# Performance work log

Measured on AMD Instinct MI355X. Metric: run time of the kernel, lower is better.

Reference implementation:

```python
import jax, jax.numpy as jnp
import numpy as np

H = 96          # hidden_dim / GatedGraphConv out_channels
L = 6           # num_layers
F_IN = 32       # num_node_features
G = 4096        # number of graphs in batch
BN_EPS = 1e-5


def setup_inputs() -> dict:
    key = jax.random.key(0)
    ks = jax.random.split(key, 16)
    N, E = 100000, 400000
    x = jax.random.normal(ks[0], (N, F_IN), dtype=jnp.float32)
    edge_index = jax.random.randint(ks[1], (2, E), 0, N, dtype=jnp.int64)
    batch = jnp.sort(jax.random.randint(ks[2], (N,), 0, G, dtype=jnp.int64))
    s = 1.0 / np.sqrt(H)
    conv_w = jax.random.uniform(ks[3], (L, H, H), jnp.float32, -s, s)
    w_ih = jax.random.uniform(ks[4], (3 * H, H), jnp.float32, -s, s)
    w_hh = jax.random.uniform(ks[5], (3 * H, H), jnp.float32, -s, s)
    b_ih = jax.random.uniform(ks[6], (3 * H,), jnp.float32, -s, s)
    b_hh = jax.random.uniform(ks[7], (3 * H,), jnp.float32, -s, s)
    bn_gamma = jnp.ones((H,), jnp.float32)
    bn_beta = jnp.zeros((H,), jnp.float32)
    s1 = 1.0 / np.sqrt(H)
    fc1_w = jax.random.uniform(ks[8], (4 * H, H), jnp.float32, -s1, s1)
    fc1_b = jax.random.uniform(ks[9], (4 * H,), jnp.float32, -s1, s1)
    s2 = 1.0 / np.sqrt(4 * H)
    fc2_w = jax.random.uniform(ks[10], (H, 4 * H), jnp.float32, -s2, s2)
    fc2_b = jax.random.uniform(ks[11], (H,), jnp.float32, -s2, s2)
    fc3_w = jax.random.uniform(ks[12], (1, H), jnp.float32, -s1, s1)
    fc3_b = jax.random.uniform(ks[13], (1,), jnp.float32, -s1, s1)
    return dict(x=x, edge_index=edge_index, batch=batch, conv_w=conv_w,
                w_ih=w_ih, w_hh=w_hh, b_ih=b_ih, b_hh=b_hh,
                bn_gamma=bn_gamma, bn_beta=bn_beta,
                fc1_w=fc1_w, fc1_b=fc1_b, fc2_w=fc2_w, fc2_b=fc2_b,
                fc3_w=fc3_w, fc3_b=fc3_b)


def _gated_graph_conv(x, src, dst, conv_w, w_ih, w_hh, b_ih, b_hh):
    N = x.shape[0]
    # PyG zero-pads input features up to out_channels
    h = jnp.pad(x, ((0, 0), (0, H - x.shape[1])))
    for i in range(L):
        m = h @ conv_w[i]                         # [N, H]
        agg = jnp.zeros((N, H), m.dtype).at[dst].add(m[src])  # scatter-add at targets
        gi = agg @ w_ih.T + b_ih                  # [N, 3H]
        gh = h @ w_hh.T + b_hh                    # [N, 3H]
        i_r, i_z, i_n = jnp.split(gi, 3, axis=-1)
        h_r, h_z, h_n = jnp.split(gh, 3, axis=-1)
        r = jax.nn.sigmoid(i_r + h_r)
        z = jax.nn.sigmoid(i_z + h_z)
        n = jnp.tanh(i_n + r * h_n)
        h = (1.0 - z) * n + z * h
    return h


def reference(x, edge_index, batch, conv_w, w_ih, w_hh, b_ih, b_hh,
              bn_gamma, bn_beta, fc1_w, fc1_b, fc2_w, fc2_b, fc3_w, fc3_b):
    src, dst = edge_index[0], edge_index[1]
    h = _gated_graph_conv(x, src, dst, conv_w, w_ih, w_hh, b_ih, b_hh)
    h = jax.nn.relu(h)
    # global mean pool (dropout is identity in eval)
    sums = jax.ops.segment_sum(h, batch, num_segments=G)          # [G, H]
    counts = jax.ops.segment_sum(jnp.ones((h.shape[0],), h.dtype), batch, num_segments=G)
    pooled = sums / jnp.maximum(counts, 1.0)[:, None]
    # BatchNorm1d in eval mode: running_mean=0, running_var=1
    hbn = (pooled / jnp.sqrt(1.0 + BN_EPS)) * bn_gamma + bn_beta
    h1 = jax.nn.relu(hbn @ fc1_w.T + fc1_b)
    h2 = jax.nn.relu(h1 @ fc2_w.T + fc2_b)
    return h2 @ fc3_w.T + fc3_b                                    # [G, 1]
```

## Files before the change

kernel.cpp:

```cpp
#include <hip/hip_runtime.h>

#define H96 96
#define LAYERS 6
#define BN_EPS 1e-5f
#define SCAN_B 1024

typedef unsigned short u16;
typedef unsigned int u32;
typedef _Float16 f16;
typedef _Float16 h8 __attribute__((ext_vector_type(8)));
typedef float f32x4 __attribute__((ext_vector_type(4)));
typedef u32 u32x3 __attribute__((ext_vector_type(3)));

__device__ __forceinline__ float sigm(float x) { return 1.f / (1.f + __expf(-x)); }
__device__ __forceinline__ float tanh_(float x) { return 2.f / (1.f + __expf(-2.f * x)) - 1.f; }
__device__ __forceinline__ f32x4 splat4(float x) { f32x4 v = {x, x, x, x}; return v; }

struct h2s { f16 x, y; };

__device__ __forceinline__ void upk(u32 v, float& lo, float& hi) {
    union { u32 u; h2s h; } c;
    c.u = v;
    lo = (float)c.h.x;
    hi = (float)c.h.y;
}

__global__ void k_f2h(const float* __restrict__ convw, const float* __restrict__ wih,
                      const float* __restrict__ whh, const float* __restrict__ fc1w,
                      const float* __restrict__ fc2w, f16* __restrict__ dst) {
    int i = blockIdx.x * 256 + threadIdx.x;
    if (i >= 184320) return;
    float v;
    if (i < 55296) v = convw[i];
    else if (i < 82944) v = wih[i - 55296];
    else if (i < 110592) v = whh[i - 82944];
    else if (i < 147456) v = fc1w[i - 110592];
    else v = fc2w[i - 147456];
    dst[i] = (f16)v;
}

__global__ __launch_bounds__(256) void k_wpt(const f16* __restrict__ wih16, const f16* __restrict__ convw16,
                                             f16* __restrict__ wpt) {
    int l = blockIdx.y;
    int lane = threadIdx.x & 63, wave = threadIdx.x >> 6;
    int l15 = lane & 15, q = lane >> 4;
    int rowa = blockIdx.x * 64 + wave * 16 + l15;
    if (rowa >= 288) rowa = 287;
    const f16* B = convw16 + (size_t)l * 9216;
    h8 af[3];
#pragma unroll
    for (int s = 0; s < 3; s++) af[s] = *(const h8*)(wih16 + (size_t)rowa * 96 + s * 32 + q * 8);
    f32x4 acc[6];
#pragma unroll
    for (int t = 0; t < 6; t++) acc[t] = splat4(0.f);
#pragma unroll
    for (int s = 0; s < 3; s++)
#pragma unroll
        for (int t = 0; t < 6; t++) {
            h8 b = *(const h8*)(B + (size_t)(t * 16 + l15) * 96 + s * 32 + q * 8);
            acc[t] = __builtin_amdgcn_mfma_f32_16x16x32_f16(af[s], b, acc[t], 0, 0, 0);
        }
    int rbase = blockIdx.x * 64 + wave * 16 + q * 4;
#pragma unroll
    for (int t = 0; t < 6; t++)
#pragma unroll
        for (int rr = 0; rr < 4; rr++) {
            int row = rbase + rr;
            if (row < 288) wpt[(size_t)l * 27648 + (size_t)row * 96 + t * 16 + l15] = (f16)acc[t][rr];
        }
}

__global__ void k_pad(const float* __restrict__ x, f16* __restrict__ hf, int N) {
    int i = blockIdx.x * 256 + threadIdx.x;
    if (i >= N * H96) return;
    int n = i / H96, c = i - n * H96;
    float v = (c < 32) ? x[n * 32 + c] : 0.f;
    hf[i] = (f16)v;
}

__global__ void k_hist(const int* __restrict__ key, int* __restrict__ deg, int E) {
    int e = blockIdx.x * 256 + threadIdx.x;
    if (e < E) atomicAdd(&deg[key[e]], 1);
}

__global__ __launch_bounds__(SCAN_B) void k_scan1(const int* __restrict__ deg, int* __restrict__ incl,
                                                  int* __restrict__ bsum, int N) {
    __shared__ int sh[SCAN_B];
    int i = blockIdx.x * SCAN_B + threadIdx.x;
    int v = (i < N) ? deg[i] : 0;
    sh[threadIdx.x] = v;
    __syncthreads();
    for (int off = 1; off < SCAN_B; off <<= 1) {
        int t = (threadIdx.x >= (u32)off) ? sh[threadIdx.x - off] : 0;
        __syncthreads();
        sh[threadIdx.x] += t;
        __syncthreads();
    }
    incl[blockIdx.x * SCAN_B + threadIdx.x] = sh[threadIdx.x];
    if (threadIdx.x == SCAN_B - 1) bsum[blockIdx.x] = sh[threadIdx.x];
}

__global__ void k_scan2(int* __restrict__ bsum, int nb) {
    if (blockIdx.x == 0 && threadIdx.x == 0) {
        int run = 0;
        for (int i = 0; i < nb; i++) { run += bsum[i]; bsum[i] = run; }
    }
}

__global__ void k_scan3(const int* __restrict__ deg, const int* __restrict__ incl, const int* __restrict__ bsum,
                        int* __restrict__ rs, int* __restrict__ cur, int N, int E) {
    int i = blockIdx.x * 256 + threadIdx.x;
    if (i == 0) rs[N] = E;
    if (i < N) {
        int b = i / SCAN_B;
        int off = (b > 0) ? bsum[b - 1] : 0;
        int ex = incl[i] - deg[i] + off;
        rs[i] = ex;
        if (cur) cur[i] = ex;
    }
}

__global__ void k_fill(const int* __restrict__ src, const int* __restrict__ dst, int* __restrict__ cur,
                       int* __restrict__ es, int E) {
    int e = blockIdx.x * 256 + threadIdx.x;
    if (e < E) {
        int p = atomicAdd(&cur[dst[e]], 1);
        es[p] = src[e];
    }
}

__global__ __launch_bounds__(256) void k_gather(const f16* __restrict__ hin, const int* __restrict__ rs,
                                                const int* __restrict__ es, f16* __restrict__ agg, int N) {
    int grp = threadIdx.x >> 4;
    int lane6 = threadIdx.x & 15;
    int node = blockIdx.x * 16 + grp;
    if (node >= N) return;
    int s = rs[node], e = rs[node + 1];
    float a0 = 0, a1 = 0, a2 = 0, a3 = 0, a4 = 0, a5 = 0;
    const char* basep = (const char*)hin;
    int off = lane6 * 12;
    for (int i = s; i < e; i += 4) {
        int j1 = (i + 1 < e) ? i + 1 : i;
        int j2 = (i + 2 < e) ? i + 2 : i;
        int j3 = (i + 3 < e) ? i + 3 : i;
        float m1 = (i + 1 < e) ? 1.f : 0.f;
        float m2 = (i + 2 < e) ? 1.f : 0.f;
        float m3 = (i + 3 < e) ? 1.f : 0.f;
        int sa = es[i], sb = es[j1], sc = es[j2], sd = es[j3];
        u32x3 va = *(const u32x3*)(basep + (size_t)sa * 192 + off);
        u32x3 vb = *(const u32x3*)(basep + (size_t)sb * 192 + off);
        u32x3 vc = *(const u32x3*)(basep + (size_t)sc * 192 + off);
        u32x3 vd = *(const u32x3*)(basep + (size_t)sd * 192 + off);
        float t0, t1;
        upk(va.x, t0, t1); a0 += t0; a1 += t1;
        upk(va.y, t0, t1); a2 += t0; a3 += t1;
        upk(va.z, t0, t1); a4 += t0; a5 += t1;
        upk(vb.x, t0, t1); a0 += t0 * m1; a1 += t1 * m1;
        upk(vb.y, t0, t1); a2 += t0 * m1; a3 += t1 * m1;
        upk(vb.z, t0, t1); a4 += t0 * m1; a5 += t1 * m1;
        upk(vc.x, t0, t1); a0 += t0 * m2; a1 += t1 * m2;
        upk(vc.y, t0, t1); a2 += t0 * m2; a3 += t1 * m2;
        upk(vc.z, t0, t1); a4 += t0 * m2; a5 += t1 * m2;
        upk(vd.x, t0, t1); a0 += t0 * m3; a1 += t1 * m3;
        upk(vd.y, t0, t1); a2 += t0 * m3; a3 += t1 * m3;
        upk(vd.z, t0, t1); a4 += t0 * m3; a5 += t1 * m3;
    }
    f16* dp = agg + (size_t)node * H96 + lane6 * 6;
    h2s p0, p1, p2;
    p0.x = (f16)a0; p0.y = (f16)a1;
    p1.x = (f16)a2; p1.y = (f16)a3;
    p2.x = (f16)a4; p2.y = (f16)a5;
    *(h2s*)(dp + 0) = p0;
    *(h2s*)(dp + 2) = p1;
    *(h2s*)(dp + 4) = p2;
}

__global__ __launch_bounds__(384, 4) void k_gru(const f16* __restrict__ agg, const f16* __restrict__ hin,
                                                f16* __restrict__ hout, const f16* __restrict__ wpt,
                                                const f16* __restrict__ whh, const float* __restrict__ bih,
                                                const float* __restrict__ bhh, int N) {
    int w = threadIdx.x >> 6;
    int lane = threadIdx.x & 63;
    int l15 = lane & 15, q = lane >> 4;
    int jr = w * 16 + l15;
    float b_r = bih[jr] + bhh[jr];
    float b_z = bih[96 + jr] + bhh[96 + jr];
    float b_in = bih[192 + jr];
    float b_hn = bhh[192 + jr];
    h8 wr0[3], wr1[3], wz0[3], wz1[3], wn0[3], wn1[3];
#pragma unroll
    for (int s = 0; s < 3; s++) {
        int ko = s * 32 + q * 8;
        wr0[s] = *(const h8*)(wpt + (size_t)jr * H96 + ko);
        wz0[s] = *(const h8*)(wpt + (size_t)(96 + jr) * H96 + ko);
        wn0[s] = *(const h8*)(wpt + (size_t)(192 + jr) * H96 + ko);
        wr1[s] = *(const h8*)(whh + (size_t)jr * H96 + ko);
        wz1[s] = *(const h8*)(whh + (size_t)(96 + jr) * H96 + ko);
        wn1[s] = *(const h8*)(whh + (size_t)(192 + jr) * H96 + ko);
    }
    int ntiles = (N + 15) >> 4;
    for (int tile = blockIdx.x; tile < ntiles; tile += gridDim.x) {
        int base = tile << 4;
        int rowa = base + l15;
        if (rowa >= N) rowa = N - 1;
        h8 as_[3], ah[3];
#pragma unroll
        for (int s = 0; s < 3; s++) {
            as_[s] = *(const h8*)(agg + (size_t)rowa * H96 + s * 32 + q * 8);
            ah[s] = *(const h8*)(hin + (size_t)rowa * H96 + s * 32 + q * 8);
        }
        f32x4 r = splat4(b_r), z = splat4(b_z), nn = splat4(b_in), hn = splat4(b_hn);
#pragma unroll
        for (int s = 0; s < 3; s++) {
            r = __builtin_amdgcn_mfma_f32_16x16x32_f16(as_[s], wr0[s], r, 0, 0, 0);
            r = __builtin_amdgcn_mfma_f32_16x16x32_f16(ah[s], wr1[s], r, 0, 0, 0);
            z = __builtin_amdgcn_mfma_f32_16x16x32_f16(as_[s], wz0[s], z, 0, 0, 0);
            z = __builtin_amdgcn_mfma_f32_16x16x32_f16(ah[s], wz1[s], z, 0, 0, 0);
            nn = __builtin_amdgcn_mfma_f32_16x16x32_f16(as_[s], wn0[s], nn, 0, 0, 0);
            hn = __builtin_amdgcn_mfma_f32_16x16x32_f16(ah[s], wn1[s], hn, 0, 0, 0);
        }
        int rbase = base + q * 4;
#pragma unroll
        for (int rr = 0; rr < 4; rr++) {
            int row = rbase + rr;
            if (row < N) {
                float rv = sigm(r[rr]);
                float zv = sigm(z[rr]);
                float nv = tanh_(nn[rr] + rv * hn[rr]);
                size_t idx = (size_t)row * H96 + w * 16 + l15;
                float hold = (float)hin[idx];
                float hnew = (1.f - zv) * nv + zv * hold;
                hout[idx] = (f16)hnew;
            }
        }
    }
}

__global__ void k_pool2(const f16* __restrict__ hf, const int* __restrict__ grs,
                        const float* __restrict__ gamma, const float* __restrict__ beta,
                        f16* __restrict__ pooled, int Gn) {
    int g = blockIdx.x;
    int c = threadIdx.x;
    if (g >= Gn || c >= H96) return;
    int s = grs[g], e = grs[g + 1];
    float sum = 0.f;
    for (int n = s; n < e; n++) sum += fmaxf((float)hf[(size_t)n * H96 + c], 0.f);
    float cnt = fmaxf((float)(e - s), 1.f);
    float val = (sum / cnt) * (gamma[c] * rsqrtf(1.f + BN_EPS)) + beta[c];
    pooled[(size_t)g * H96 + c] = (f16)val;
}

template <int KS, int NT, int OUTW, bool RELU>
__global__ __launch_bounds__(256) void k_mlp(const f16* __restrict__ A, const f16* __restrict__ W,
                                             const float* __restrict__ bias, f16* __restrict__ out, int M) {
    int lane = threadIdx.x & 63, wave = threadIdx.x >> 6;
    int l15 = lane & 15, q = lane >> 4;
    int colBase = blockIdx.y * (NT * 16);
    int tile = blockIdx.x;
    int rowa = tile * 64 + wave * 16 + l15;
    if (rowa >= M) rowa = M - 1;
    h8 af[KS];
#pragma unroll
    for (int s = 0; s < KS; s++) af[s] = *(const h8*)(A + (size_t)rowa * (KS * 32) + s * 32 + q * 8);
    f32x4 acc[NT];
#pragma unroll
    for (int t = 0; t < NT; t++) acc[t] = splat4(0.f);
#pragma unroll
    for (int s = 0; s < KS; s++)
#pragma unroll
        for (int t = 0; t < NT; t++) {
            h8 b = *(const h8*)(W + (size_t)(colBase + t * 16 + l15) * (KS * 32) + s * 32 + q * 8);
            acc[t] = __builtin_amdgcn_mfma_f32_16x16x32_f16(af[s], b, acc[t], 0, 0, 0);
        }
    int rbase = tile * 64 + wave * 16 + q * 4;
#pragma unroll
    for (int t = 0; t < NT; t++) {
        float bv = bias[colBase + t * 16 + l15];
#pragma unroll
        for (int rr = 0; rr < 4; rr++) {
            int row = rbase + rr;
            if (row >= M) continue;
            float v = acc[t][rr] + bv;
            if (RELU) v = fmaxf(v, 0.f);
            out[(size_t)row * OUTW + colBase + t * 16 + l15] = (f16)v;
        }
    }
}

__global__ void k_mlp3(const f16* __restrict__ h2, const float* __restrict__ w, const float* __restrict__ b,
                       float* __restrict__ out, int M) {
    int g = blockIdx.x * 256 + threadIdx.x;
    if (g >= M) return;
    float acc = 0.f;
    for (int k = 0; k < H96; k++) acc += (float)h2[(size_t)g * H96 + k] * w[k];
    out[g] = acc + b[0];
}

extern "C" void kernel_launch(void* const* d_in, const int* in_sizes, int n_in, void* d_out, int out_size,
                              void* d_ws, size_t ws_size, hipStream_t stream) {
    const float* x = (const float*)d_in[0];
    const int* ei = (const int*)d_in[1];
    const int* batch = (const int*)d_in[2];
    const float* conv_w = (const float*)d_in[3];
    const float* wih = (const float*)d_in[4];
    const float* whh = (const float*)d_in[5];
    const float* bih = (const float*)d_in[6];
    const float* bhh = (const float*)d_in[7];
    const float* gamma = (const float*)d_in[8];
    const float* beta = (const float*)d_in[9];
    const float* fc1w = (const float*)d_in[10];
    const float* fc1b = (const float*)d_in[11];
    const float* fc2w = (const float*)d_in[12];
    const float* fc2b = (const float*)d_in[13];
    const float* fc3w = (const float*)d_in[14];
    const float* fc3b = (const float*)d_in[15];

    int N = in_sizes[0] / 32;
    int E = in_sizes[1] / 2;
    int Gn = out_size;
    const int* srcp = ei;
    const int* dstp = ei + E;

    char* p = (char*)d_ws;
    auto alloc = [&](size_t bytes) -> char* {
        char* r = p;
        p += (bytes + 255) & ~(size_t)255;
        return r;
    };
    f16* hA = (f16*)alloc((size_t)N * H96 * 2);
    f16* hB = (f16*)alloc((size_t)N * H96 * 2);
    f16* aggf = (f16*)alloc((size_t)N * H96 * 2);
    f16* wf16 = (f16*)alloc((size_t)184320 * 2);
    f16* wpt = (f16*)alloc((size_t)LAYERS * 27648 * 2);
    int nb = (N + SCAN_B - 1) / SCAN_B;
    int* deg = (int*)alloc((size_t)N * 4);
    int* incl = (int*)alloc((size_t)nb * SCAN_B * 4);
    int* bsum = (int*)alloc((size_t)nb * 4);
    int* rs = (int*)alloc((size_t)(N + 1) * 4);
    int* cur = (int*)alloc((size_t)N * 4);
    int* es = (int*)alloc((size_t)E * 4);
    int nb2 = (Gn + SCAN_B - 1) / SCAN_B;
    int* gdeg = (int*)alloc((size_t)Gn * 4);
    int* gincl = (int*)alloc((size_t)nb2 * SCAN_B * 4);
    int* gbsum = (int*)alloc((size_t)nb2 * 4);
    int* grs = (int*)alloc((size_t)(Gn + 1) * 4);
    f16* pooled = (f16*)alloc((size_t)Gn * H96 * 2);
    f16* h1 = (f16*)alloc((size_t)Gn * 384 * 2);
    f16* h2 = (f16*)alloc((size_t)Gn * H96 * 2);

    f16* convw16 = wf16;
    f16* wih16 = wf16 + 55296;
    f16* whh16 = wf16 + 82944;
    f16* fc1w16 = wf16 + 110592;
    f16* fc2w16 = wf16 + 147456;

    hipMemsetAsync(deg, 0, (size_t)N * 4, stream);
    hipMemsetAsync(gdeg, 0, (size_t)Gn * 4, stream);

    k_f2h<<<720, 256, 0, stream>>>(conv_w, wih, whh, fc1w, fc2w, wf16);
    k_wpt<<<dim3(5, 6), 256, 0, stream>>>(wih16, convw16, wpt);
    k_pad<<<(N * H96 + 255) / 256, 256, 0, stream>>>(x, hA, N);
    k_hist<<<(E + 255) / 256, 256, 0, stream>>>(dstp, deg, E);
    k_scan1<<<nb, SCAN_B, 0, stream>>>(deg, incl, bsum, N);
    k_scan2<<<1, 64, 0, stream>>>(bsum, nb);
    k_scan3<<<(N + 255) / 256, 256, 0, stream>>>(deg, incl, bsum, rs, cur, N, E);
    k_fill<<<(E + 255) / 256, 256, 0, stream>>>(srcp, dstp, cur, es, E);
    k_hist<<<(N + 255) / 256, 256, 0, stream>>>(batch, gdeg, N);
    k_scan1<<<nb2, SCAN_B, 0, stream>>>(gdeg, gincl, gbsum, Gn);
    k_scan2<<<1, 64, 0, stream>>>(gbsum, nb2);
    k_scan3<<<(Gn + 255) / 256, 256, 0, stream>>>(gdeg, gincl, gbsum, grs, (int*)nullptr, Gn, N);

    int nt16 = (N + 15) / 16;
    for (int l = 0; l < LAYERS; l++) {
        f16* hin = (l & 1) ? hB : hA;
        f16* hout = (l & 1) ? hA : hB;
        k_gather<<<nt16, 256, 0, stream>>>(hin, rs, es, aggf, N);
        k_gru<<<1280, 384, 0, stream>>>(aggf, hin, hout, wpt + (size_t)l * 27648, whh16, bih, bhh, N);
    }

    k_pool2<<<Gn, 128, 0, stream>>>(hA, grs, gamma, beta, pooled, Gn);
    k_mlp<3, 6, 384, true><<<dim3((Gn + 63) / 64, 4), 256, 0, stream>>>(pooled, fc1w16, fc1b, h1, Gn);
    k_mlp<12, 6, 96, true><<<dim3((Gn + 63) / 64, 1), 256, 0, stream>>>(h1, fc2w16, fc2b, h2, Gn);
    k_mlp3<<<(Gn + 255) / 256, 256, 0, stream>>>(h2, fc3w, fc3b, (float*)d_out, Gn);
}
```

Baseline: 557.9 us.

## Software-pipeline GRU tile loads with register prefetch and fewer persistent blocks

The GRU kernel now loads the next tile's agg and h fragments into registers while computing the current tile, double-buffering the operand fetches to hide global-memory latency behind the MFMAs. Weights are held as f32x4 and pinned in VGPRs with an empty asm barrier so the compiler cannot rematerialize or spill them. Launch bounds drop to 2 blocks per SIMD target and the grid shrinks from 1280 to 512 blocks, so each block processes more tiles. The extra registers for prefetch reduce occupancy, and fewer blocks may leave some CUs underused.

```diff
diff --git a/kernel.cpp b/kernel.cpp
--- a/kernel.cpp
+++ b/kernel.cpp
@@ -15,6 +15,7 @@
 __device__ __forceinline__ float sigm(float x) { return 1.f / (1.f + __expf(-x)); }
 __device__ __forceinline__ float tanh_(float x) { return 2.f / (1.f + __expf(-2.f * x)) - 1.f; }
 __device__ __forceinline__ f32x4 splat4(float x) { f32x4 v = {x, x, x, x}; return v; }
+__device__ __forceinline__ h8 H8(f32x4 v) { return __builtin_bit_cast(h8, v); }
 
 struct h2s { f16 x, y; };
 
@@ -175,7 +176,7 @@
     *(h2s*)(dp + 4) = p2;
 }
 
-__global__ __launch_bounds__(384, 4) void k_gru(const f16* __restrict__ agg, const f16* __restrict__ hin,
+__global__ __launch_bounds__(384, 2) void k_gru(const f16* __restrict__ agg, const f16* __restrict__ hin,
                                                 f16* __restrict__ hout, const f16* __restrict__ wpt,
                                                 const f16* __restrict__ whh, const float* __restrict__ bih,
                                                 const float* __restrict__ bhh, int N) {
@@ -187,38 +188,61 @@
     float b_z = bih[96 + jr] + bhh[96 + jr];
     float b_in = bih[192 + jr];
     float b_hn = bhh[192 + jr];
-    h8 wr0[3], wr1[3], wz0[3], wz1[3], wn0[3], wn1[3];
+    f32x4 wr0[3], wr1[3], wz0[3], wz1[3], wn0[3], wn1[3];
 #pragma unroll
     for (int s = 0; s < 3; s++) {
         int ko = s * 32 + q * 8;
-        wr0[s] = *(const h8*)(wpt + (size_t)jr * H96 + ko);
-        wz0[s] = *(const h8*)(wpt + (size_t)(96 + jr) * H96 + ko);
-        wn0[s] = *(const h8*)(wpt + (size_t)(192 + jr) * H96 + ko);
-        wr1[s] = *(const h8*)(whh + (size_t)jr * H96 + ko);
-        wz1[s] = *(const h8*)(whh + (size_t)(96 + jr) * H96 + ko);
-        wn1[s] = *(const h8*)(whh + (size_t)(192 + jr) * H96 + ko);
-    }
+        wr0[s] = *(const f32x4*)(wpt + (size_t)jr * H96 + ko);
+        wz0[s] = *(const f32x4*)(wpt + (size_t)(96 + jr) * H96 + ko);
+        wn0[s] = *(const f32x4*)(wpt + (size_t)(192 + jr) * H96 + ko);
+        wr1[s] = *(const f32x4*)(whh + (size_t)jr * H96 + ko);
+        wz1[s] = *(const f32x4*)(whh + (size_t)(96 + jr) * H96 + ko);
+        wn1[s] = *(const f32x4*)(whh + (size_t)(192 + jr) * H96 + ko);
+    }
+#pragma unroll
+    for (int s = 0; s < 3; s++) {
+        asm volatile("" : "+v"(wr0[s]), "+v"(wr1[s]), "+v"(wz0[s]), "+v"(wz1[s]), "+v"(wn0[s]), "+v"(wn1[s]));
+    }
+
     int ntiles = (N + 15) >> 4;
-    for (int tile = blockIdx.x; tile < ntiles; tile += gridDim.x) {
-        int base = tile << 4;
-        int rowa = base + l15;
+    int stride = gridDim.x;
+    int tile = blockIdx.x;
+    if (tile >= ntiles) return;
+
+    h8 as_[3], ah[3];
+    {
+        int rowa = (tile << 4) + l15;
         if (rowa >= N) rowa = N - 1;
-        h8 as_[3], ah[3];
 #pragma unroll
         for (int s = 0; s < 3; s++) {
             as_[s] = *(const h8*)(agg + (size_t)rowa * H96 + s * 32 + q * 8);
             ah[s] = *(const h8*)(hin + (size_t)rowa * H96 + s * 32 + q * 8);
         }
+    }
+    while (true) {
+        int nxt = tile + stride;
+        int lt = (nxt < ntiles) ? nxt : tile;
+        h8 as2[3], ah2[3];
+        {
+            int rowa = (lt << 4) + l15;
+            if (rowa >= N) rowa = N - 1;
+#pragma unroll
+            for (int s = 0; s < 3; s++) {
+                as2[s] = *(const h8*)(agg + (size_t)rowa * H96 + s * 32 + q * 8);
+                ah2[s] = *(const h8*)(hin + (size_t)rowa * H96 + s * 32 + q * 8);
+            }
+        }
         f32x4 r = splat4(b_r), z = splat4(b_z), nn = splat4(b_in), hn = splat4(b_hn);
 #pragma unroll
         for (int s = 0; s < 3; s++) {
-            r = __builtin_amdgcn_mfma_f32_16x16x32_f16(as_[s], wr0[s], r, 0, 0, 0);
-            r = __builtin_amdgcn_mfma_f32_16x16x32_f16(ah[s], wr1[s], r, 0, 0, 0);
-            z = __builtin_amdgcn_mfma_f32_16x16x32_f16(as_[s], wz0[s], z, 0, 0, 0);
-            z = __builtin_amdgcn_mfma_f32_16x16x32_f16(ah[s], wz1[s], z, 0, 0, 0);
-            nn = __builtin_amdgcn_mfma_f32_16x16x32_f16(as_[s], wn0[s], nn, 0, 0, 0);
-            hn = __builtin_amdgcn_mfma_f32_16x16x32_f16(ah[s], wn1[s], hn, 0, 0, 0);
-        }
+            r = __builtin_amdgcn_mfma_f32_16x16x32_f16(as_[s], H8(wr0[s]), r, 0, 0, 0);
+            r = __builtin_amdgcn_mfma_f32_16x16x32_f16(ah[s], H8(wr1[s]), r, 0, 0, 0);
+            z = __builtin_amdgcn_mfma_f32_16x16x32_f16(as_[s], H8(wz0[s]), z, 0, 0, 0);
+            z = __builtin_amdgcn_mfma_f32_16x16x32_f16(ah[s], H8(wz1[s]), z, 0, 0, 0);
+            nn = __builtin_amdgcn_mfma_f32_16x16x32_f16(as_[s], H8(wn0[s]), nn, 0, 0, 0);
+            hn = __builtin_amdgcn_mfma_f32_16x16x32_f16(ah[s], H8(wn1[s]), hn, 0, 0, 0);
+        }
+        int base = tile << 4;
         int rbase = base + q * 4;
 #pragma unroll
         for (int rr = 0; rr < 4; rr++) {
@@ -232,6 +256,13 @@
                 float hnew = (1.f - zv) * nv + zv * hold;
                 hout[idx] = (f16)hnew;
             }
+        }
+        if (nxt >= ntiles) break;
+        tile = nxt;
+#pragma unroll
+        for (int s = 0; s < 3; s++) {
+            as_[s] = as2[s];
+            ah[s] = ah2[s];
         }
     }
 }
@@ -375,7 +406,7 @@
         f16* hin = (l & 1) ? hB : hA;
         f16* hout = (l & 1) ? hA : hB;
         k_gather<<<nt16, 256, 0, stream>>>(hin, rs, es, aggf, N);
-        k_gru<<<1280, 384, 0, stream>>>(aggf, hin, hout, wpt + (size_t)l * 27648, whh16, bih, bhh, N);
+        k_gru<<<512, 384, 0, stream>>>(aggf, hin, hout, wpt + (size_t)l * 27648, whh16, bih, bhh, N);
     }
 
     k_pool2<<<Gn, 128, 0, stream>>>(hA, grs, gamma, beta, pooled, Gn);
```

Measured after the change: 590.3 us. 1.06x slower.
